# Kernel tuning notes

Hardware: AMD Instinct MI355X
Metric: run time of the kernel (lower is better)

## Reference

```python
import jax, jax.numpy as jnp
import numpy as np

B, S, D = 4, 512, 256

def setup_inputs() -> dict:
    key = jax.random.key(0)
    ks = jax.random.split(key, 32)
    def w(k, shape, s=0.05):
        return jax.random.normal(k, shape, dtype=jnp.float32) * s
    inp = {
        "img": jax.random.normal(ks[0], (B, S, D), dtype=jnp.float32),
        "audio": jax.random.normal(ks[1], (B, S, D), dtype=jnp.float32),
        "common": jax.random.normal(ks[2], (B, S, D), dtype=jnp.float32),
    }
    names = ["qv", "qa", "kv", "ka", "cc", "w5", "w6", "w7", "w8"]
    for i, n in enumerate(names):
        inp[n + "_w"] = w(ks[3 + 2 * i], (D, D))   # stored [in, out]
        inp[n + "_b"] = w(ks[4 + 2 * i], (D,))
    inp["bil_w"] = w(ks[25], (D, D, D))            # Bilinear weight [out, in1, in2]
    inp["t_o"] = jnp.ones((), dtype=jnp.float32)
    return inp


def reference(img, audio, common,
              qv_w, qv_b, qa_w, qa_b, kv_w, kv_b, ka_w, ka_b, cc_w, cc_b,
              w5_w, w5_b, w6_w, w6_b, w7_w, w7_b, w8_w, w8_b,
              bil_w, t_o):
    dim_k = qv_w.shape[1]
    norm_fact = 1.0 / jnp.sqrt(jnp.asarray(dim_k, dtype=jnp.float32))

    lin = lambda x, w, b: x @ w + b
    # NOTE: faithful to source - softmax first, THEN scaled by norm_fact.
    attn = lambda q, k: jax.nn.softmax(jnp.einsum('bsd,btd->bst', q, k), axis=-1) * norm_fact

    W_q_v = lin(img, qv_w, qv_b)
    W_q_a = lin(audio, qa_w, qa_b)
    w_k_a = lin(audio, ka_w, ka_b)
    W_k_v = lin(img, kv_w, kv_b)
    C_c = lin(common, cc_w, cc_b)

    atten_vv = attn(W_q_v, W_k_v)
    atten_vc = attn(W_q_v, C_c)
    atten_aa = attn(W_q_a, w_k_a)
    atten_ac = attn(W_q_a, C_c)

    vc_common = jnp.einsum('bst,btd->bsd', atten_vc, common)
    ac_common = jnp.einsum('bst,btd->bsd', atten_ac, common)

    common_feat_v = (1.0 + lin(vc_common, w5_w, w5_b)) * jnp.einsum('bst,btd->bsd', atten_vv, img) + lin(vc_common, w6_w, w6_b)
    common_feat_a = (1.0 + lin(ac_common, w7_w, w7_b)) * jnp.einsum('bst,btd->bsd', atten_aa, audio) + lin(ac_common, w8_w, w8_b)

    # Bilinear: out[b,s,k] = v[b,s,:] @ W[k] @ a[b,s,:]
    atten_m = jnp.einsum('bsi,kij,bsj->bsk', common_feat_v, bil_w, common_feat_a)
    j_o = jax.nn.sigmoid(atten_m)
    Z_k_o = t_o * j_o * img + (1.0 - j_o) * audio
    return (Z_k_o + img, Z_k_o + audio)
```

## Files before the change

kernel.cpp:

```cpp
#include <hip/hip_runtime.h>
#include <hip/hip_bf16.h>

typedef unsigned short ushortT;
typedef __bf16 bf16x8 __attribute__((ext_vector_type(8)));
typedef float f32x4 __attribute__((ext_vector_type(4)));
typedef ushortT ush8 __attribute__((ext_vector_type(8)));
typedef ushortT ush4 __attribute__((ext_vector_type(4)));

#define MFMA16(a, b, c) __builtin_amdgcn_mfma_f32_16x16x32_bf16((a), (b), (c), 0, 0, 0)

__device__ __forceinline__ ushortT f2b(float f) {
  __hip_bfloat16 h = __float2bfloat16(f);
  return __builtin_bit_cast(ushortT, h);
}
__device__ __forceinline__ float b2f(ushortT u) {
  __hip_bfloat16 h = __builtin_bit_cast(__hip_bfloat16, u);
  return __bfloat162float(h);
}

__device__ __forceinline__ void async16(const void* g, void* l) {
  __builtin_amdgcn_global_load_lds((const __attribute__((address_space(1))) unsigned int*)g,
                                   (__attribute__((address_space(3))) unsigned int*)l, 16, 0, 0);
}

__device__ __forceinline__ bf16x8 scale8(bf16x8 a, float s) {
  union { bf16x8 v; unsigned int u[4]; } in, out;
  in.v = a;
#pragma unroll
  for (int p = 0; p < 4; p++) {
    float lo = __builtin_bit_cast(float, in.u[p] << 16);
    float hi = __builtin_bit_cast(float, in.u[p] & 0xffff0000u);
    lo *= s;
    hi *= s;
    unsigned int r;
    asm("v_cvt_pk_bf16_f32 %0, %1, %2" : "=v"(r) : "v"(lo), "v"(hi));
    out.u[p] = r;
  }
  return out.v;
}

#define ACT_E 524288
#define WD_E  65536

#define OFF_ACT16   0u
#define OFF_ACTT16  3145728u
#define OFF_W16T    6291456u
#define OFF_PROJ16  7471104u
#define OFF_P16     12713984u
#define OFF_VC16    21102592u
#define OFF_AC16    22151168u
#define OFF_PVV32   23199744u
#define OFF_PVA32   25296896u
#define OFF_PART    0u
#define OFF_BIL16   33554432u
#define OFF_CFV16   67108864u
#define OFF_CFA16   68157440u

__global__ void k_cvt_acts(const float* __restrict__ img, const float* __restrict__ aud,
                           const float* __restrict__ com, ushortT* __restrict__ dst) {
  int i4 = blockIdx.x * 256 + threadIdx.x;
#pragma unroll
  for (int q = 0; q < 4; q++) {
    int idx4 = i4 + q * 98304;
    int flat = idx4 * 4;
    const float* src;
    int off;
    if (flat < 524288)        { src = img; off = flat; }
    else if (flat < 1048576)  { src = aud; off = flat - 524288; }
    else                      { src = com; off = flat - 1048576; }
    float4 v = *(const float4*)(src + off);
    ush4 u = { f2b(v.x), f2b(v.y), f2b(v.z), f2b(v.w) };
    *(ush4*)(dst + idx4 * 4) = u;
  }
}

__global__ void k_cvt_bil(const float* __restrict__ bil, ushortT* __restrict__ dst) {
  int i4 = blockIdx.x * 256 + threadIdx.x;
#pragma unroll
  for (int q = 0; q < 8; q++) {
    int idx4 = i4 + q * 524288;
    float4 v = *(const float4*)(bil + idx4 * 4);
    ush4 u = { f2b(v.x), f2b(v.y), f2b(v.z), f2b(v.w) };
    *(ush4*)(dst + idx4 * 4) = u;
  }
}

__global__ void k_transpose(const float* __restrict__ img, const float* __restrict__ aud,
                            const float* __restrict__ com,
                            const float* w0, const float* w1, const float* w2,
                            const float* w3, const float* w4, const float* w5,
                            const float* w6, const float* w7, const float* w8,
                            ushortT* __restrict__ actT, ushortT* __restrict__ wT) {
  __shared__ ushortT tl[64][72];
  int tid = threadIdx.x;
  int bx = blockIdx.x;
  const float* src;
  ushortT* dst;
  int R, C, r0, c0;
  if (bx < 384) {
    int inst = bx >> 5, tile = bx & 31;
    int act = inst >> 2, bb = inst & 3;
    src = (act == 0 ? img : (act == 1 ? aud : com)) + bb * 131072;
    dst = actT + act * 524288 + bb * 131072;
    R = 512; C = 256;
    r0 = (tile >> 2) * 64; c0 = (tile & 3) * 64;
  } else {
    int bw = bx - 384;
    int w = bw >> 4, tile = bw & 15;
    const float* s;
    switch (w) {
      case 0: s = w0; break; case 1: s = w1; break; case 2: s = w2; break;
      case 3: s = w3; break; case 4: s = w4; break; case 5: s = w5; break;
      case 6: s = w6; break; case 7: s = w7; break; default: s = w8; break;
    }
    src = s;
    dst = wT + w * 65536;
    R = 256; C = 256;
    r0 = (tile >> 2) * 64; c0 = (tile & 3) * 64;
  }
#pragma unroll
  for (int q = 0; q < 4; q++) {
    int rr = q * 16 + (tid >> 4);
    int cs = (tid & 15) * 4;
    float4 v = *(const float4*)(src + (r0 + rr) * C + c0 + cs);
    tl[rr][cs + 0] = f2b(v.x);
    tl[rr][cs + 1] = f2b(v.y);
    tl[rr][cs + 2] = f2b(v.z);
    tl[rr][cs + 3] = f2b(v.w);
  }
  __syncthreads();
#pragma unroll
  for (int q = 0; q < 4; q++) {
    int cc = q * 16 + (tid >> 4);
    int rs = (tid & 15) * 4;
    ush4 u = { tl[rs + 0][cc], tl[rs + 1][cc], tl[rs + 2][cc], tl[rs + 3][cc] };
    *(ush4*)(dst + (c0 + cc) * R + r0 + rs) = u;
  }
}

__global__ __launch_bounds__(512) void k_linear5(
    const ushortT* __restrict__ act16, const ushortT* __restrict__ wT,
    const float* __restrict__ b0, const float* __restrict__ b1,
    const float* __restrict__ b2, const float* __restrict__ b3,
    const float* __restrict__ b4, ushortT* __restrict__ proj16) {
  __shared__ ushortT Al[4][32][8];
  __shared__ ushortT Bl[4][256][8];
  const int tid = threadIdx.x, l = tid & 63, w = tid >> 6;
  const int bx = blockIdx.x;
  const int op = bx >> 6, sblk = bx & 63;
  const int s0 = sblk * 32;
  const int xsel = (op == 4) ? 2 : (op & 1);
  const ushortT* X = act16 + xsel * ACT_E;
  const ushortT* W = wT + op * WD_E;
  const float* bias = op == 0 ? b0 : op == 1 ? b1 : op == 2 ? b2 : op == 3 ? b3 : b4;
  ushortT* out = proj16 + op * ACT_E;

  f32x4 acc[2][2] = {};
  ush8 ra, rb[2];
  int a_row = tid >> 2, a_seg = tid & 3;

  auto sload = [&](int k0) {
    if (tid < 128) ra = *(const ush8*)(X + (s0 + a_row) * 256 + k0 + a_seg * 8);
#pragma unroll
    for (int q = 0; q < 2; q++) {
      int slot = tid + q * 512;
      rb[q] = *(const ush8*)(W + (slot >> 2) * 256 + k0 + (slot & 3) * 8);
    }
  };
  auto swrite = [&]() {
    if (tid < 128) *(ush8*)(&Al[a_seg][a_row][0]) = ra;
#pragma unroll
    for (int q = 0; q < 2; q++) {
      int slot = tid + q * 512;
      *(ush8*)(&Bl[slot & 3][slot >> 2][0]) = rb[q];
    }
  };

  sload(0); swrite(); __syncthreads();
  for (int s = 0; s < 8; s++) {
    if (s < 7) sload((s + 1) * 32);
    int ks = l >> 4;
    bf16x8 a[2], bb[2];
#pragma unroll
    for (int m = 0; m < 2; m++) a[m] = *(const bf16x8*)(&Al[ks][m * 16 + (l & 15)][0]);
#pragma unroll
    for (int n = 0; n < 2; n++) bb[n] = *(const bf16x8*)(&Bl[ks][w * 32 + n * 16 + (l & 15)][0]);
#pragma unroll
    for (int m = 0; m < 2; m++)
#pragma unroll
      for (int n = 0; n < 2; n++) acc[m][n] = MFMA16(a[m], bb[n], acc[m][n]);
    if (s == 7) break;
    __syncthreads();
    swrite();
    __syncthreads();
  }
#pragma unroll
  for (int m = 0; m < 2; m++)
#pragma unroll
    for (int n = 0; n < 2; n++)
#pragma unroll
      for (int r = 0; r < 4; r++) {
        int row = s0 + m * 16 + (l >> 4) * 4 + r;
        int col = w * 32 + n * 16 + (l & 15);
        out[row * 256 + col] = f2b(acc[m][n][r] + bias[col]);
      }
}

__global__ __launch_bounds__(512) void k_attn(const ushortT* __restrict__ proj16,
                                              ushortT* __restrict__ P16) {
  __shared__ ushortT Ql[8][4][32][8];
  __shared__ ushortT Kl[4][512][8];
  __shared__ float red[32][8];
  const int tid = threadIdx.x, l = tid & 63, w = tid >> 6;
  const int bx = blockIdx.x;
  const int p = bx >> 6, b = (bx >> 4) & 3, sblk = bx & 15;
  const int s0 = sblk * 32;
  const int qsel = (p < 2) ? 0 : 1;
  const int ksel = (p == 0) ? 2 : (p == 2) ? 3 : 4;
  const ushortT* Q = proj16 + qsel * ACT_E + b * 131072;
  const ushortT* K = proj16 + ksel * ACT_E + b * 131072;
  ushortT* P = P16 + p * 1048576 + b * 262144;

#pragma unroll
  for (int q = 0; q < 2; q++) {
    int slot = tid + q * 512;
    int row = slot >> 5, seg = slot & 31;
    ush8 v = *(const ush8*)(Q + (s0 + row) * 256 + seg * 8);
    *(ush8*)(&Ql[seg >> 2][seg & 3][row][0]) = v;
  }

  f32x4 acc[2][4] = {};
  ush8 rk[4];
  auto kload = [&](int d0) {
#pragma unroll
    for (int q = 0; q < 4; q++) {
      int slot = tid + q * 512;
      rk[q] = *(const ush8*)(K + (slot >> 2) * 256 + d0 + (slot & 3) * 8);
    }
  };
  auto kwrite = [&]() {
#pragma unroll
    for (int q = 0; q < 4; q++) {
      int slot = tid + q * 512;
      *(ush8*)(&Kl[slot & 3][slot >> 2][0]) = rk[q];
    }
  };

  kload(0); kwrite(); __syncthreads();
  for (int s = 0; s < 8; s++) {
    if (s < 7) kload((s + 1) * 32);
    int ks = l >> 4;
    bf16x8 a[2], bb[4];
#pragma unroll
    for (int m = 0; m < 2; m++) a[m] = *(const bf16x8*)(&Ql[s][ks][m * 16 + (l & 15)][0]);
#pragma unroll
    for (int n = 0; n < 4; n++) bb[n] = *(const bf16x8*)(&Kl[ks][w * 64 + n * 16 + (l & 15)][0]);
#pragma unroll
    for (int m = 0; m < 2; m++)
#pragma unroll
      for (int n = 0; n < 4; n++) acc[m][n] = MFMA16(a[m], bb[n], acc[m][n]);
    if (s == 7) break;
    __syncthreads();
    kwrite();
    __syncthreads();
  }

  float gmax[2][4];
#pragma unroll
  for (int m = 0; m < 2; m++)
#pragma unroll
    for (int r = 0; r < 4; r++) {
      float v = fmaxf(fmaxf(acc[m][0][r], acc[m][1][r]), fmaxf(acc[m][2][r], acc[m][3][r]));
#pragma unroll
      for (int off = 1; off < 16; off <<= 1) v = fmaxf(v, __shfl_xor(v, off, 16));
      if ((l & 15) == 0) red[m * 16 + (l >> 4) * 4 + r][w] = v;
    }
  __syncthreads();
#pragma unroll
  for (int m = 0; m < 2; m++)
#pragma unroll
    for (int r = 0; r < 4; r++) {
      int sr = m * 16 + (l >> 4) * 4 + r;
      float g = red[sr][0];
#pragma unroll
      for (int ww = 1; ww < 8; ww++) g = fmaxf(g, red[sr][ww]);
      gmax[m][r] = g;
    }
  __syncthreads();
#pragma unroll
  for (int m = 0; m < 2; m++)
#pragma unroll
    for (int r = 0; r < 4; r++) {
      float ssum = 0.f;
#pragma unroll
      for (int n = 0; n < 4; n++) {
        float e = __expf(acc[m][n][r] - gmax[m][r]);
        acc[m][n][r] = e;
        ssum += e;
      }
#pragma unroll
      for (int off = 1; off < 16; off <<= 1) ssum += __shfl_xor(ssum, off, 16);
      if ((l & 15) == 0) red[m * 16 + (l >> 4) * 4 + r][w] = ssum;
    }
  __syncthreads();
#pragma unroll
  for (int m = 0; m < 2; m++)
#pragma unroll
    for (int r = 0; r < 4; r++) {
      int sr = m * 16 + (l >> 4) * 4 + r;
      float tot = 0.f;
#pragma unroll
      for (int ww = 0; ww < 8; ww++) tot += red[sr][ww];
      float sc = 0.0625f / tot;
#pragma unroll
      for (int n = 0; n < 4; n++)
        P[(s0 + sr) * 512 + w * 64 + n * 16 + (l & 15)] = f2b(acc[m][n][r] * sc);
    }
}

__global__ __launch_bounds__(512) void k_pv(const ushortT* __restrict__ P16,
                                            const ushortT* __restrict__ actT,
                                            float* __restrict__ pvv, float* __restrict__ pva,
                                            ushortT* __restrict__ vc16, ushortT* __restrict__ ac16) {
  __shared__ ushortT Al[4][32][8];
  __shared__ ushortT Bl[4][256][8];
  const int tid = threadIdx.x, l = tid & 63, w = tid >> 6;
  const int bx = blockIdx.x;
  const int p = bx >> 6, b = (bx >> 4) & 3, sblk = bx & 15;
  const int s0 = sblk * 32;
  const ushortT* A = P16 + p * 1048576 + b * 262144;
  const int vsel = (p == 0) ? 0 : (p == 2) ? 1 : 2;
  const ushortT* VT = actT + vsel * ACT_E + b * 131072;

  f32x4 acc[2][2] = {};
  ush8 ra, rb[2];
  int a_row = tid >> 2, a_seg = tid & 3;
  auto sload = [&](int t0) {
    if (tid < 128) ra = *(const ush8*)(A + (s0 + a_row) * 512 + t0 + a_seg * 8);
#pragma unroll
    for (int q = 0; q < 2; q++) {
      int slot = tid + q * 512;
      rb[q] = *(const ush8*)(VT + (slot >> 2) * 512 + t0 + (slot & 3) * 8);
    }
  };
  auto swrite = [&]() {
    if (tid < 128) *(ush8*)(&Al[a_seg][a_row][0]) = ra;
#pragma unroll
    for (int q = 0; q < 2; q++) {
      int slot = tid + q * 512;
      *(ush8*)(&Bl[slot & 3][slot >> 2][0]) = rb[q];
    }
  };

  sload(0); swrite(); __syncthreads();
  for (int s = 0; s < 16; s++) {
    if (s < 15) sload((s + 1) * 32);
    int ks = l >> 4;
    bf16x8 a[2], bb[2];
#pragma unroll
    for (int m = 0; m < 2; m++) a[m] = *(const bf16x8*)(&Al[ks][m * 16 + (l & 15)][0]);
#pragma unroll
    for (int n = 0; n < 2; n++) bb[n] = *(const bf16x8*)(&Bl[ks][w * 32 + n * 16 + (l & 15)][0]);
#pragma unroll
    for (int m = 0; m < 2; m++)
#pragma unroll
      for (int n = 0; n < 2; n++) acc[m][n] = MFMA16(a[m], bb[n], acc[m][n]);
    if (s == 15) break;
    __syncthreads();
    swrite();
    __syncthreads();
  }
#pragma unroll
  for (int m = 0; m < 2; m++)
#pragma unroll
    for (int n = 0; n < 2; n++)
#pragma unroll
      for (int r = 0; r < 4; r++) {
        int row = s0 + m * 16 + (l >> 4) * 4 + r;
        int col = w * 32 + n * 16 + (l & 15);
        int gi = (b * 512 + row) * 256 + col;
        float v = acc[m][n][r];
        if (p == 0) pvv[gi] = v;
        else if (p == 1) vc16[gi] = f2b(v);
        else if (p == 2) pva[gi] = v;
        else ac16[gi] = f2b(v);
      }
}

__global__ __launch_bounds__(512) void k_lin4c(
    const ushortT* __restrict__ vc16, const ushortT* __restrict__ ac16,
    const ushortT* __restrict__ wT,
    const float* __restrict__ w5b, const float* __restrict__ w6b,
    const float* __restrict__ w7b, const float* __restrict__ w8b,
    const float* __restrict__ pvv, const float* __restrict__ pva,
    ushortT* __restrict__ cfv, ushortT* __restrict__ cfa) {
  __shared__ ushortT Al[4][32][8];
  __shared__ ushortT B1[4][256][8];
  __shared__ ushortT B2[4][256][8];
  const int tid = threadIdx.x, l = tid & 63, w = tid >> 6;
  const int bx = blockIdx.x;
  const int side = bx >> 6, sblk = bx & 63;
  const int s0 = sblk * 32;
  const ushortT* A = side ? ac16 : vc16;
  const ushortT* W1 = wT + (side ? 7 : 5) * WD_E;
  const ushortT* W2 = wT + (side ? 8 : 6) * WD_E;
  const float* bb1 = side ? w7b : w5b;
  const float* bb2 = side ? w8b : w6b;
  const float* pv = side ? pva : pvv;
  ushortT* out = side ? cfa : cfv;

  f32x4 acc1[2][2] = {}, acc2[2][2] = {};
  ush8 ra, rb1[2], rb2[2];
  int a_row = tid >> 2, a_seg = tid & 3;
  auto sload = [&](int k0) {
    if (tid < 128) ra = *(const ush8*)(A + (s0 + a_row) * 256 + k0 + a_seg * 8);
#pragma unroll
    for (int q = 0; q < 2; q++) {
      int slot = tid + q * 512;
      rb1[q] = *(const ush8*)(W1 + (slot >> 2) * 256 + k0 + (slot & 3) * 8);
      rb2[q] = *(const ush8*)(W2 + (slot >> 2) * 256 + k0 + (slot & 3) * 8);
    }
  };
  auto swrite = [&]() {
    if (tid < 128) *(ush8*)(&Al[a_seg][a_row][0]) = ra;
#pragma unroll
    for (int q = 0; q < 2; q++) {
      int slot = tid + q * 512;
      *(ush8*)(&B1[slot & 3][slot >> 2][0]) = rb1[q];
      *(ush8*)(&B2[slot & 3][slot >> 2][0]) = rb2[q];
    }
  };

  sload(0); swrite(); __syncthreads();
  for (int s = 0; s < 8; s++) {
    if (s < 7) sload((s + 1) * 32);
    int ks = l >> 4;
    bf16x8 a[2], x1[2], x2[2];
#pragma unroll
    for (int m = 0; m < 2; m++) a[m] = *(const bf16x8*)(&Al[ks][m * 16 + (l & 15)][0]);
#pragma unroll
    for (int n = 0; n < 2; n++) {
      x1[n] = *(const bf16x8*)(&B1[ks][w * 32 + n * 16 + (l & 15)][0]);
      x2[n] = *(const bf16x8*)(&B2[ks][w * 32 + n * 16 + (l & 15)][0]);
    }
#pragma unroll
    for (int m = 0; m < 2; m++)
#pragma unroll
      for (int n = 0; n < 2; n++) {
        acc1[m][n] = MFMA16(a[m], x1[n], acc1[m][n]);
        acc2[m][n] = MFMA16(a[m], x2[n], acc2[m][n]);
      }
    if (s == 7) break;
    __syncthreads();
    swrite();
    __syncthreads();
  }
#pragma unroll
  for (int m = 0; m < 2; m++)
#pragma unroll
    for (int n = 0; n < 2; n++)
#pragma unroll
      for (int r = 0; r < 4; r++) {
        int row = s0 + m * 16 + (l >> 4) * 4 + r;
        int col = w * 32 + n * 16 + (l & 15);
        int gi = row * 256 + col;
        float u1 = acc1[m][n][r] + bb1[col];
        float u2 = acc2[m][n][r] + bb2[col];
        out[gi] = f2b((1.f + u1) * pv[gi] + u2);
      }
}

__global__ __launch_bounds__(512, 1) void k_bilinear8(
    const ushortT* __restrict__ cfa, const ushortT* __restrict__ cfv,
    const ushortT* __restrict__ W, ushortT* __restrict__ part) {
  __shared__ char arena[140288];
  const int tid = threadIdx.x, l = tid & 63, w = tid >> 6;
  const int d = blockIdx.x;
  const int L = (d & 7) * 32 + (d >> 3);
  const int ic = L >> 3;
  const int mb = L & 7;
  const int r0 = mb * 256;
  const int icb = ic * 8;
  const int wr = w >> 1, wc = w & 1;

  float* cfvl = (float*)(arena + 131072);
  if (tid < 256) {
    ush8 v = *(const ush8*)(cfv + (size_t)(r0 + tid) * 256 + icb);
    float* dp = cfvl + tid * 9;
#pragma unroll
    for (int q = 0; q < 8; q++) dp[q] = b2f(v[q]);
  }

  int pS[4], aOff[4], bOff[4], cvIdx[4];
#pragma unroll
  for (int s = 0; s < 4; s++) {
    int p = (tid + s * 512) * 16;
    int lg = p ^ (((p >> 7) & 7) << 4);
    int row = lg >> 7, colb = lg & 127;
    pS[s] = p;
    cvIdx[s] = row * 9;
    aOff[s] = (r0 + row) * 512 + colb;
    bOff[s] = row * 131072 + icb * 512 + colb;
  }
  const char* cfaB = (const char*)cfa;
  const char* WB = (const char*)W;

  int aoff[2][4], boff[2][8];
#pragma unroll
  for (int m = 0; m < 4; m++) {
    int row = wr * 64 + m * 16 + (l & 15);
    int b0 = row * 128 + (l >> 4) * 16;
    int msk = (row & 7) << 4;
    aoff[0][m] = b0 ^ msk;
    aoff[1][m] = (b0 + 64) ^ msk;
  }
#pragma unroll
  for (int n = 0; n < 8; n++) {
    int row = wc * 128 + n * 16 + (l & 15);
    int b0 = row * 128 + (l >> 4) * 16;
    int msk = (row & 7) << 4;
    boff[0][n] = b0 ^ msk;
    boff[1][n] = (b0 + 64) ^ msk;
  }

  ush8 arg[4];
  auto loadA = [&](int t) {
    int ja = (t & 3) << 7;
#pragma unroll
    for (int s = 0; s < 4; s++) arg[s] = *(const ush8*)(cfaB + aOff[s] + ja);
  };
  auto gloadB = [&](int t, char* Bb) {
    int jb = ((t >> 2) << 9) + ((t & 3) << 7);
#pragma unroll
    for (int s = 0; s < 4; s++) async16(WB + bOff[s] + jb, Bb + pS[s]);
  };
  auto writeA = [&](int t, char* Ab) {
    int ii = t >> 2;
#pragma unroll
    for (int s = 0; s < 4; s++) {
      float sc = cfvl[cvIdx[s] + ii];
      *(bf16x8*)(Ab + pS[s]) = scale8(__builtin_bit_cast(bf16x8, arg[s]), sc);
    }
  };

  f32x4 macc[4][8] = {};

  loadA(0);
  gloadB(0, arena + 65536);
  __syncthreads();
  writeA(0, arena);
  __syncthreads();

  for (int t = 0; t < 32; t++) {
    char* Ab = arena + ((t & 1) << 15);
    char* Bb = arena + 65536 + ((t & 1) << 15);
    char* An = arena + (((t + 1) & 1) << 15);
    char* Bn = arena + 65536 + (((t + 1) & 1) << 15);

    bf16x8 a0[4];
#pragma unroll
    for (int m = 0; m < 4; m++) a0[m] = *(const bf16x8*)(Ab + aoff[0][m]);

    if (t < 31) { loadA(t + 1); gloadB(t + 1, Bn); }

    {
      bf16x8 bl[4];
#pragma unroll
      for (int n = 0; n < 4; n++) bl[n] = *(const bf16x8*)(Bb + boff[0][n]);
      __builtin_amdgcn_s_setprio(1);
#pragma unroll
      for (int m = 0; m < 4; m++)
#pragma unroll
        for (int n = 0; n < 4; n++) macc[m][n] = MFMA16(a0[m], bl[n], macc[m][n]);
      __builtin_amdgcn_s_setprio(0);
    }
    {
      bf16x8 bh[4];
#pragma unroll
      for (int n = 0; n < 4; n++) bh[n] = *(const bf16x8*)(Bb + boff[0][n + 4]);
      __builtin_amdgcn_s_setprio(1);
#pragma unroll
      for (int m = 0; m < 4; m++)
#pragma unroll
        for (int n = 0; n < 4; n++) macc[m][n + 4] = MFMA16(a0[m], bh[n], macc[m][n + 4]);
      __builtin_amdgcn_s_setprio(0);
    }

    if (t < 31) writeA(t + 1, An);

    bf16x8 a1[4];
#pragma unroll
    for (int m = 0; m < 4; m++) a1[m] = *(const bf16x8*)(Ab + aoff[1][m]);
    {
      bf16x8 bl[4];
#pragma unroll
      for (int n = 0; n < 4; n++) bl[n] = *(const bf16x8*)(Bb + boff[1][n]);
      __builtin_amdgcn_s_setprio(1);
#pragma unroll
      for (int m = 0; m < 4; m++)
#pragma unroll
        for (int n = 0; n < 4; n++) macc[m][n] = MFMA16(a1[m], bl[n], macc[m][n]);
      __builtin_amdgcn_s_setprio(0);
    }
    {
      bf16x8 bh[4];
#pragma unroll
      for (int n = 0; n < 4; n++) bh[n] = *(const bf16x8*)(Bb + boff[1][n + 4]);
      __builtin_amdgcn_s_setprio(1);
#pragma unroll
      for (int m = 0; m < 4; m++)
#pragma unroll
        for (int n = 0; n < 4; n++) macc[m][n + 4] = MFMA16(a1[m], bh[n], macc[m][n + 4]);
      __builtin_amdgcn_s_setprio(0);
    }

    __syncthreads();
  }

  ushortT* dst = part + (size_t)ic * 524288 + (size_t)r0 * 256;
#pragma unroll
  for (int m = 0; m < 4; m++)
#pragma unroll
    for (int n = 0; n < 8; n++)
#pragma unroll
      for (int r = 0; r < 4; r++)
        dst[(wr * 64 + m * 16 + ((l >> 4) << 2) + r) * 256 + wc * 128 + n * 16 + (l & 15)] =
            f2b(macc[m][n][r]);
}

__global__ void k_final2(const ushortT* __restrict__ part, const float* __restrict__ img,
                         const float* __restrict__ aud, const float* __restrict__ t_o,
                         float* __restrict__ out0, float* __restrict__ out1) {
  int i = blockIdx.x * 256 + threadIdx.x;
  float t = t_o[0];
  float4 m = {0.f, 0.f, 0.f, 0.f};
#pragma unroll
  for (int ic = 0; ic < 32; ic++) {
    ush4 p = *(const ush4*)(part + (size_t)ic * 524288 + (size_t)i * 4);
    m.x += b2f(p[0]); m.y += b2f(p[1]); m.z += b2f(p[2]); m.w += b2f(p[3]);
  }
  float4 a = ((const float4*)img)[i];
  float4 u = ((const float4*)aud)[i];
  float4 o0, o1;
  {
    float j = 1.f / (1.f + __expf(-m.x)); float Z = t * j * a.x + (1.f - j) * u.x;
    o0.x = Z + a.x; o1.x = Z + u.x;
  }
  {
    float j = 1.f / (1.f + __expf(-m.y)); float Z = t * j * a.y + (1.f - j) * u.y;
    o0.y = Z + a.y; o1.y = Z + u.y;
  }
  {
    float j = 1.f / (1.f + __expf(-m.z)); float Z = t * j * a.z + (1.f - j) * u.z;
    o0.z = Z + a.z; o1.z = Z + u.z;
  }
  {
    float j = 1.f / (1.f + __expf(-m.w)); float Z = t * j * a.w + (1.f - j) * u.w;
    o0.w = Z + a.w; o1.w = Z + u.w;
  }
  ((float4*)out0)[i] = o0;
  ((float4*)out1)[i] = o1;
}

extern "C" void kernel_launch(void* const* d_in, const int* in_sizes, int n_in,
                              void* d_out, int out_size, void* d_ws, size_t ws_size,
                              hipStream_t stream) {
  const float* img   = (const float*)d_in[0];
  const float* aud   = (const float*)d_in[1];
  const float* com   = (const float*)d_in[2];
  const float* qv_w  = (const float*)d_in[3];
  const float* qv_b  = (const float*)d_in[4];
  const float* qa_w  = (const float*)d_in[5];
  const float* qa_b  = (const float*)d_in[6];
  const float* kv_w  = (const float*)d_in[7];
  const float* kv_b  = (const float*)d_in[8];
  const float* ka_w  = (const float*)d_in[9];
  const float* ka_b  = (const float*)d_in[10];
  const float* cc_w  = (const float*)d_in[11];
  const float* cc_b  = (const float*)d_in[12];
  const float* w5_w  = (const float*)d_in[13];
  const float* w5_b  = (const float*)d_in[14];
  const float* w6_w  = (const float*)d_in[15];
  const float* w6_b  = (const float*)d_in[16];
  const float* w7_w  = (const float*)d_in[17];
  const float* w7_b  = (const float*)d_in[18];
  const float* w8_w  = (const float*)d_in[19];
  const float* w8_b  = (const float*)d_in[20];
  const float* bil_w = (const float*)d_in[21];
  const float* t_o   = (const float*)d_in[22];
  float* out = (float*)d_out;

  char* ws = (char*)d_ws;
  ushortT* act16  = (ushortT*)(ws + OFF_ACT16);
  ushortT* actT16 = (ushortT*)(ws + OFF_ACTT16);
  ushortT* w16t   = (ushortT*)(ws + OFF_W16T);
  ushortT* proj16 = (ushortT*)(ws + OFF_PROJ16);
  ushortT* P16    = (ushortT*)(ws + OFF_P16);
  ushortT* vc16   = (ushortT*)(ws + OFF_VC16);
  ushortT* ac16   = (ushortT*)(ws + OFF_AC16);
  float*   pvv32  = (float*)(ws + OFF_PVV32);
  float*   pva32  = (float*)(ws + OFF_PVA32);
  ushortT* part   = (ushortT*)(ws + OFF_PART);
  ushortT* bil16  = (ushortT*)(ws + OFF_BIL16);
  ushortT* cfv16  = (ushortT*)(ws + OFF_CFV16);
  ushortT* cfa16  = (ushortT*)(ws + OFF_CFA16);

  k_cvt_acts<<<384, 256, 0, stream>>>(img, aud, com, act16);
  k_cvt_bil<<<2048, 256, 0, stream>>>(bil_w, bil16);
  k_transpose<<<528, 256, 0, stream>>>(img, aud, com, qv_w, qa_w, kv_w, ka_w, cc_w,
                                       w5_w, w6_w, w7_w, w8_w, actT16, w16t);
  k_linear5<<<320, 512, 0, stream>>>(act16, w16t, qv_b, qa_b, kv_b, ka_b, cc_b, proj16);
  k_attn<<<256, 512, 0, stream>>>(proj16, P16);
  k_pv<<<256, 512, 0, stream>>>(P16, actT16, pvv32, pva32, vc16, ac16);
  k_lin4c<<<128, 512, 0, stream>>>(vc16, ac16, w16t, w5_b, w6_b, w7_b, w8_b,
                                   pvv32, pva32, cfv16, cfa16);
  k_bilinear8<<<256, 512, 0, stream>>>(cfa16, cfv16, bil16, part);
  k_final2<<<512, 256, 0, stream>>>(part, img, aud, t_o, out, out + 524288);
}
```

Measured before the change: 148.4 us.

## Fuse attention softmax with PV matmul and merge prep conversion kernels

The three preprocessing kernels (activation cast, bilinear weight cast, transposes) are merged into one launch, with the row-major bf16 activation copy written from the transpose pass. The attention kernel now keeps the normalized probability tile in shared memory and immediately multiplies it by V, so the separate PV kernel and the global round trip of the P matrix go away. The cost is a larger shared-memory arena (about 81 KB) that lowers occupancy and adds aliasing between the Q and V regions, plus one fewer launch boundary to hide latency.

```diff
diff --git a/kernel.cpp b/kernel.cpp
--- a/kernel.cpp
+++ b/kernel.cpp
@@ -56,52 +56,38 @@
 #define OFF_CFV16   67108864u
 #define OFF_CFA16   68157440u
 
-__global__ void k_cvt_acts(const float* __restrict__ img, const float* __restrict__ aud,
-                           const float* __restrict__ com, ushortT* __restrict__ dst) {
-  int i4 = blockIdx.x * 256 + threadIdx.x;
-#pragma unroll
-  for (int q = 0; q < 4; q++) {
-    int idx4 = i4 + q * 98304;
-    int flat = idx4 * 4;
-    const float* src;
-    int off;
-    if (flat < 524288)        { src = img; off = flat; }
-    else if (flat < 1048576)  { src = aud; off = flat - 524288; }
-    else                      { src = com; off = flat - 1048576; }
-    float4 v = *(const float4*)(src + off);
-    ush4 u = { f2b(v.x), f2b(v.y), f2b(v.z), f2b(v.w) };
-    *(ush4*)(dst + idx4 * 4) = u;
-  }
-}
-
-__global__ void k_cvt_bil(const float* __restrict__ bil, ushortT* __restrict__ dst) {
-  int i4 = blockIdx.x * 256 + threadIdx.x;
-#pragma unroll
-  for (int q = 0; q < 8; q++) {
-    int idx4 = i4 + q * 524288;
-    float4 v = *(const float4*)(bil + idx4 * 4);
-    ush4 u = { f2b(v.x), f2b(v.y), f2b(v.z), f2b(v.w) };
-    *(ush4*)(dst + idx4 * 4) = u;
-  }
-}
-
-__global__ void k_transpose(const float* __restrict__ img, const float* __restrict__ aud,
-                            const float* __restrict__ com,
-                            const float* w0, const float* w1, const float* w2,
-                            const float* w3, const float* w4, const float* w5,
-                            const float* w6, const float* w7, const float* w8,
-                            ushortT* __restrict__ actT, ushortT* __restrict__ wT) {
-  __shared__ ushortT tl[64][72];
+__global__ void k_prep(const float* __restrict__ img, const float* __restrict__ aud,
+                       const float* __restrict__ com,
+                       const float* w0, const float* w1, const float* w2,
+                       const float* w3, const float* w4, const float* w5,
+                       const float* w6, const float* w7, const float* w8,
+                       const float* __restrict__ bil,
+                       ushortT* __restrict__ act16, ushortT* __restrict__ actT,
+                       ushortT* __restrict__ wT, ushortT* __restrict__ bil16) {
   int tid = threadIdx.x;
   int bx = blockIdx.x;
+  if (bx >= 528) {
+    int i4 = (bx - 528) * 256 + tid;
+#pragma unroll
+    for (int q = 0; q < 8; q++) {
+      int idx4 = i4 + q * 524288;
+      float4 v = *(const float4*)(bil + (size_t)idx4 * 4);
+      ush4 u = { f2b(v.x), f2b(v.y), f2b(v.z), f2b(v.w) };
+      *(ush4*)(bil16 + (size_t)idx4 * 4) = u;
+    }
+    return;
+  }
+  __shared__ ushortT tl[64][72];
   const float* src;
   ushortT* dst;
-  int R, C, r0, c0;
+  ushortT* lin = nullptr;
+  int C, r0, c0, R;
   if (bx < 384) {
     int inst = bx >> 5, tile = bx & 31;
     int act = inst >> 2, bb = inst & 3;
     src = (act == 0 ? img : (act == 1 ? aud : com)) + bb * 131072;
     dst = actT + act * 524288 + bb * 131072;
+    lin = act16 + act * 524288 + bb * 131072;
     R = 512; C = 256;
     r0 = (tile >> 2) * 64; c0 = (tile & 3) * 64;
   } else {
@@ -123,10 +109,12 @@
     int rr = q * 16 + (tid >> 4);
     int cs = (tid & 15) * 4;
     float4 v = *(const float4*)(src + (r0 + rr) * C + c0 + cs);
-    tl[rr][cs + 0] = f2b(v.x);
-    tl[rr][cs + 1] = f2b(v.y);
-    tl[rr][cs + 2] = f2b(v.z);
-    tl[rr][cs + 3] = f2b(v.w);
+    ush4 u = { f2b(v.x), f2b(v.y), f2b(v.z), f2b(v.w) };
+    tl[rr][cs + 0] = u[0];
+    tl[rr][cs + 1] = u[1];
+    tl[rr][cs + 2] = u[2];
+    tl[rr][cs + 3] = u[3];
+    if (lin) *(ush4*)(lin + (r0 + rr) * 256 + c0 + cs) = u;
   }
   __syncthreads();
 #pragma unroll
@@ -206,20 +194,27 @@
       }
 }
 
-__global__ __launch_bounds__(512) void k_attn(const ushortT* __restrict__ proj16,
-                                              ushortT* __restrict__ P16) {
-  __shared__ ushortT Ql[8][4][32][8];
-  __shared__ ushortT Kl[4][512][8];
-  __shared__ float red[32][8];
+__global__ __launch_bounds__(512) void k_attnpv(
+    const ushortT* __restrict__ proj16, const ushortT* __restrict__ actT,
+    float* __restrict__ pvv, float* __restrict__ pva,
+    ushortT* __restrict__ vc16, ushortT* __restrict__ ac16) {
+  __shared__ char arena[82944];
+  auto Ql = (ushortT(*)[4][32][8])(arena);
+  auto Kl = (ushortT(*)[512][8])(arena + 16384);
+  auto Pl = (ushortT(*)[4][32][8])(arena + 49152);
+  auto Vl = (ushortT(*)[256][8])(arena);
+  auto red = (float(*)[8])(arena + 81920);
+
   const int tid = threadIdx.x, l = tid & 63, w = tid >> 6;
   const int bx = blockIdx.x;
   const int p = bx >> 6, b = (bx >> 4) & 3, sblk = bx & 15;
   const int s0 = sblk * 32;
   const int qsel = (p < 2) ? 0 : 1;
   const int ksel = (p == 0) ? 2 : (p == 2) ? 3 : 4;
+  const int vsel = (p == 0) ? 0 : (p == 2) ? 1 : 2;
   const ushortT* Q = proj16 + qsel * ACT_E + b * 131072;
   const ushortT* K = proj16 + ksel * ACT_E + b * 131072;
-  ushortT* P = P16 + p * 1048576 + b * 262144;
+  const ushortT* VT = actT + vsel * ACT_E + b * 131072;
 
 #pragma unroll
   for (int q = 0; q < 2; q++) {
@@ -313,61 +308,49 @@
       for (int ww = 0; ww < 8; ww++) tot += red[sr][ww];
       float sc = 0.0625f / tot;
 #pragma unroll
-      for (int n = 0; n < 4; n++)
-        P[(s0 + sr) * 512 + w * 64 + n * 16 + (l & 15)] = f2b(acc[m][n][r] * sc);
-    }
-}
-
-__global__ __launch_bounds__(512) void k_pv(const ushortT* __restrict__ P16,
-                                            const ushortT* __restrict__ actT,
-                                            float* __restrict__ pvv, float* __restrict__ pva,
-                                            ushortT* __restrict__ vc16, ushortT* __restrict__ ac16) {
-  __shared__ ushortT Al[4][32][8];
-  __shared__ ushortT Bl[4][256][8];
-  const int tid = threadIdx.x, l = tid & 63, w = tid >> 6;
-  const int bx = blockIdx.x;
-  const int p = bx >> 6, b = (bx >> 4) & 3, sblk = bx & 15;
-  const int s0 = sblk * 32;
-  const ushortT* A = P16 + p * 1048576 + b * 262144;
-  const int vsel = (p == 0) ? 0 : (p == 2) ? 1 : 2;
-  const ushortT* VT = actT + vsel * ACT_E + b * 131072;
-
-  f32x4 acc[2][2] = {};
-  ush8 ra, rb[2];
-  int a_row = tid >> 2, a_seg = tid & 3;
-  auto sload = [&](int t0) {
-    if (tid < 128) ra = *(const ush8*)(A + (s0 + a_row) * 512 + t0 + a_seg * 8);
+      for (int n = 0; n < 4; n++) {
+        int S = w * 2 + (n >> 1);
+        int KS = ((n & 1) << 1) | ((l & 15) >> 3);
+        Pl[S][KS][sr][l & 7] = f2b(acc[m][n][r] * sc);
+      }
+    }
+
+  f32x4 acc2[2][2] = {};
+  ush8 rv[2];
+  auto vload = [&](int t0) {
 #pragma unroll
     for (int q = 0; q < 2; q++) {
       int slot = tid + q * 512;
-      rb[q] = *(const ush8*)(VT + (slot >> 2) * 512 + t0 + (slot & 3) * 8);
-    }
-  };
-  auto swrite = [&]() {
-    if (tid < 128) *(ush8*)(&Al[a_seg][a_row][0]) = ra;
+      rv[q] = *(const ush8*)(VT + (slot >> 2) * 512 + t0 + (slot & 3) * 8);
+    }
+  };
+  auto vwrite = [&]() {
 #pragma unroll
     for (int q = 0; q < 2; q++) {
       int slot = tid + q * 512;
-      *(ush8*)(&Bl[slot & 3][slot >> 2][0]) = rb[q];
-    }
-  };
-
-  sload(0); swrite(); __syncthreads();
+      *(ush8*)(&Vl[slot & 3][slot >> 2][0]) = rv[q];
+    }
+  };
+
+  vload(0);
+  __syncthreads();
+  vwrite();
+  __syncthreads();
   for (int s = 0; s < 16; s++) {
-    if (s < 15) sload((s + 1) * 32);
+    if (s < 15) vload((s + 1) * 32);
     int ks = l >> 4;
     bf16x8 a[2], bb[2];
 #pragma unroll
-    for (int m = 0; m < 2; m++) a[m] = *(const bf16x8*)(&Al[ks][m * 16 + (l & 15)][0]);
-#pragma unroll
-    for (int n = 0; n < 2; n++) bb[n] = *(const bf16x8*)(&Bl[ks][w * 32 + n * 16 + (l & 15)][0]);
+    for (int m = 0; m < 2; m++) a[m] = *(const bf16x8*)(&Pl[s][ks][m * 16 + (l & 15)][0]);
+#pragma unroll
+    for (int n = 0; n < 2; n++) bb[n] = *(const bf16x8*)(&Vl[ks][w * 32 + n * 16 + (l & 15)][0]);
 #pragma unroll
     for (int m = 0; m < 2; m++)
 #pragma unroll
-      for (int n = 0; n < 2; n++) acc[m][n] = MFMA16(a[m], bb[n], acc[m][n]);
+      for (int n = 0; n < 2; n++) acc2[m][n] = MFMA16(a[m], bb[n], acc2[m][n]);
     if (s == 15) break;
     __syncthreads();
-    swrite();
+    vwrite();
     __syncthreads();
   }
 #pragma unroll
@@ -379,7 +362,7 @@
         int row = s0 + m * 16 + (l >> 4) * 4 + r;
         int col = w * 32 + n * 16 + (l & 15);
         int gi = (b * 512 + row) * 256 + col;
-        float v = acc[m][n][r];
+        float v = acc2[m][n][r];
         if (p == 0) pvv[gi] = v;
         else if (p == 1) vc16[gi] = f2b(v);
         else if (p == 2) pva[gi] = v;
@@ -695,7 +678,6 @@
   ushortT* actT16 = (ushortT*)(ws + OFF_ACTT16);
   ushortT* w16t   = (ushortT*)(ws + OFF_W16T);
   ushortT* proj16 = (ushortT*)(ws + OFF_PROJ16);
-  ushortT* P16    = (ushortT*)(ws + OFF_P16);
   ushortT* vc16   = (ushortT*)(ws + OFF_VC16);
   ushortT* ac16   = (ushortT*)(ws + OFF_AC16);
   float*   pvv32  = (float*)(ws + OFF_PVV32);
@@ -705,13 +687,11 @@
   ushortT* cfv16  = (ushortT*)(ws + OFF_CFV16);
   ushortT* cfa16  = (ushortT*)(ws + OFF_CFA16);
 
-  k_cvt_acts<<<384, 256, 0, stream>>>(img, aud, com, act16);
-  k_cvt_bil<<<2048, 256, 0, stream>>>(bil_w, bil16);
-  k_transpose<<<528, 256, 0, stream>>>(img, aud, com, qv_w, qa_w, kv_w, ka_w, cc_w,
-                                       w5_w, w6_w, w7_w, w8_w, actT16, w16t);
+  k_prep<<<2576, 256, 0, stream>>>(img, aud, com, qv_w, qa_w, kv_w, ka_w, cc_w,
+                                   w5_w, w6_w, w7_w, w8_w, bil_w,
+                                   act16, actT16, w16t, bil16);
   k_linear5<<<320, 512, 0, stream>>>(act16, w16t, qv_b, qa_b, kv_b, ka_b, cc_b, proj16);
-  k_attn<<<256, 512, 0, stream>>>(proj16, P16);
-  k_pv<<<256, 512, 0, stream>>>(P16, actT16, pvv32, pva32, vc16, ac16);
+  k_attnpv<<<256, 512, 0, stream>>>(proj16, actT16, pvv32, pva32, vc16, ac16);
   k_lin4c<<<128, 512, 0, stream>>>(vc16, ac16, w16t, w5_b, w6_b, w7_b, w8_b,
                                    pvv32, pva32, cfv16, cfa16);
   k_bilinear8<<<256, 512, 0, stream>>>(cfa16, cfv16, bil16, part);
```

New measurement: 137.1 us (median of 2 runs). -7.6%, faster.
